# Performance work log

Measured on AMD Instinct MI355X. Metric: run time of the kernel, lower is better.

The kernel has to match this reference:

```python
import jax, jax.numpy as jnp
import numpy as np

D_MODEL = 1024
N_HEADS = 16
D_HEAD = D_MODEL // N_HEADS
IGNORE = -100000.0


def setup_inputs() -> dict:
    key = jax.random.key(0)
    ks = jax.random.split(key, 12)
    B, S = 4, 2048
    x_q = jax.random.normal(ks[0], (B, S, D_MODEL), dtype=jnp.float32)
    x_kv = jax.random.normal(ks[1], (B, S, D_MODEL), dtype=jnp.float32)
    # mask[q, k] == True means the score is replaced with IGNORE (masked out)
    mask = jax.random.randint(ks[2], (S, S), 0, 2) == 1
    sq = 1.0 / np.sqrt(D_MODEL)
    sh = 1.0 / np.sqrt(D_HEAD)
    W_Q = jax.random.normal(ks[3], (N_HEADS, D_MODEL, D_HEAD), dtype=jnp.float32) * sq
    W_K = jax.random.normal(ks[4], (N_HEADS, D_MODEL, D_HEAD), dtype=jnp.float32) * sq
    W_V = jax.random.normal(ks[5], (N_HEADS, D_MODEL, D_HEAD), dtype=jnp.float32) * sq
    W_O = jax.random.normal(ks[6], (N_HEADS, D_HEAD, D_MODEL), dtype=jnp.float32) * sh
    b_Q = jnp.zeros((N_HEADS, D_HEAD), dtype=jnp.float32)
    b_K = jnp.zeros((N_HEADS, D_HEAD), dtype=jnp.float32)
    b_V = jnp.zeros((N_HEADS, D_HEAD), dtype=jnp.float32)
    b_O = jnp.zeros((D_MODEL,), dtype=jnp.float32)
    return {"x_q": x_q, "x_kv": x_kv, "mask": mask,
            "W_Q": W_Q, "W_K": W_K, "W_V": W_V, "W_O": W_O,
            "b_Q": b_Q, "b_K": b_K, "b_V": b_V, "b_O": b_O}


def reference(x_q, x_kv, mask, W_Q, W_K, W_V, W_O, b_Q, b_K, b_V, b_O):
    # per-head QKV projections: b s d, n d h -> b s n h
    q = jnp.einsum('bsd,ndh->bsnh', x_q, W_Q) + b_Q
    k = jnp.einsum('bsd,ndh->bsnh', x_kv, W_K) + b_K
    v = jnp.einsum('bsd,ndh->bsnh', x_kv, W_V) + b_V
    scale = 1.0 / np.sqrt(D_HEAD)  # flex_attention default scaling
    # scores: [B, H, Sq, Sk]
    scores = jnp.einsum('bqnh,bknh->bnqk', q, k) * scale
    # score_mod: where mask True -> IGNORE
    scores = jnp.where(mask[None, None, :, :], jnp.float32(IGNORE), scores)
    attn = jax.nn.softmax(scores, axis=-1)
    z = jnp.einsum('bnqk,bknh->bqnh', attn, v)  # [B, Sq, H, Dh]
    # per-head output projection then sum over heads
    out = jnp.einsum('bqnh,nhd->bqd', z, W_O) + b_O
    return (out, z)
```

## Files before the change

### kernel.cpp

```cpp
#include <hip/hip_runtime.h>

#define S_LEN 2048
#define NHEAD 16
#define DHEAD 64
#define DMODEL 1024
#define BATCH 4
#define SC2 0.18033688011112042f

typedef short bf16x8 __attribute__((ext_vector_type(8)));
typedef float f32x4 __attribute__((ext_vector_type(4)));
typedef unsigned short u16;
typedef unsigned short u16x8 __attribute__((ext_vector_type(8)));
typedef unsigned short u16x4 __attribute__((ext_vector_type(4)));
typedef unsigned long long u64;

__device__ __forceinline__ u16 f2b(float f) {
  unsigned u = __builtin_bit_cast(unsigned, f);
  u += 0x7FFFu + ((u >> 16) & 1u);
  return (u16)(u >> 16);
}
__device__ __forceinline__ float b2f(u16 v) {
  unsigned u = ((unsigned)v) << 16;
  return __builtin_bit_cast(float, u);
}
__device__ __forceinline__ f32x4 mfma16(bf16x8 a, bf16x8 b, f32x4 c) {
  return __builtin_amdgcn_mfma_f32_16x16x32_bf16(a, b, c, 0, 0, 0);
}
__device__ __forceinline__ void load_lds16(const void* g, void* l) {
  __builtin_amdgcn_global_load_lds(
      (const __attribute__((address_space(1))) unsigned int*)g,
      (__attribute__((address_space(3))) unsigned int*)l, 16, 0, 0);
}
__device__ __forceinline__ float fexp2(float x) {
  return __builtin_exp2f(x);
}
__device__ __forceinline__ unsigned cvtpk(float lo, float hi) {
  unsigned r;
  asm("v_cvt_pk_bf16_f32 %0, %1, %2" : "=v"(r) : "v"(lo), "v"(hi));
  return r;
}


__global__ void cvt_f32_bf16(const float* __restrict__ src, u16* __restrict__ dst, int n4) {
  int i = blockIdx.x * 256 + threadIdx.x;
  int stride = gridDim.x * 256;
  for (; i < n4; i += stride) {
    float4 v = ((const float4*)src)[i];
    u16x4 o = { f2b(v.x), f2b(v.y), f2b(v.z), f2b(v.w) };
    ((u16x4*)dst)[i] = o;
  }
}

__global__ void mask_bits(const int* __restrict__ M, u64* __restrict__ Mbit) {
  const int tid = threadIdx.x;
  int W = blockIdx.x * 4 + (tid >> 6);
  int lane = tid & 63;
  int q = W >> 5, wo = W & 31;
  int v = M[(size_t)q * S_LEN + wo * 64 + lane];
  u64 bits = __ballot(v != 0);
  if (lane == 0) Mbit[W] = bits;
}

__global__ void repack_w(const float* __restrict__ W, u16* __restrict__ WT, float scale) {
  __shared__ u16 t[64][66];
  const int tid = threadIdx.x;
  const int n = blockIdx.y, d0 = blockIdx.x * 64;
  const float* src = W + (size_t)n * 65536;
  for (int p = 0; p < 4; ++p) {
    int idx = p * 256 + tid;
    int r = idx >> 4, cs = idx & 15;
    float4 v = *(const float4*)(src + (size_t)(d0 + r) * 64 + cs * 4);
    t[r][cs*4+0] = f2b(v.x*scale); t[r][cs*4+1] = f2b(v.y*scale);
    t[r][cs*4+2] = f2b(v.z*scale); t[r][cs*4+3] = f2b(v.w*scale);
  }
  __syncthreads();
  for (int p = 0; p < 2; ++p) {
    int idx = p * 256 + tid;
    int hl = idx >> 3, ds = idx & 7;
    u16x8 o;
    for (int e = 0; e < 8; ++e) o[e] = t[ds*8+e][hl];
    *(u16x8*)(WT + (size_t)(n*64 + hl) * 1024 + d0 + ds*8) = o;
  }
}

__global__ void split_wo(const float* __restrict__ Wo, u16* __restrict__ Hi, u16* __restrict__ Lo) {
  __shared__ u16 th[64][66];
  __shared__ u16 tl[64][66];
  const int tid = threadIdx.x;
  const int d0 = blockIdx.x * 64, c0 = blockIdx.y * 64;
  for (int p = 0; p < 4; ++p) {
    int idx = p * 256 + tid;
    int r = idx >> 4, cs = idx & 15;
    float4 v = *(const float4*)(Wo + (size_t)(c0 + r) * 1024 + d0 + cs * 4);
    float f[4] = {v.x, v.y, v.z, v.w};
    for (int e = 0; e < 4; ++e) {
      u16 hb = f2b(f[e]);
      th[r][cs*4+e] = hb;
      tl[r][cs*4+e] = f2b(f[e] - b2f(hb));
    }
  }
  __syncthreads();
  for (int p = 0; p < 2; ++p) {
    int idx = p * 256 + tid;
    int dr = idx >> 3, cs = idx & 7;
    u16x8 oh, ol;
    for (int e = 0; e < 8; ++e) { oh[e] = th[cs*8+e][dr]; ol[e] = tl[cs*8+e][dr]; }
    *(u16x8*)(Hi + (size_t)(d0 + dr) * 1024 + c0 + cs*8) = oh;
    *(u16x8*)(Lo + (size_t)(d0 + dr) * 1024 + c0 + cs*8) = ol;
  }
}

__global__ void transpose_v(const u16* __restrict__ V, u16* __restrict__ VT) {
  __shared__ u16 t[64][66];
  const int tid = threadIdx.x;
  const int s0 = blockIdx.x * 64;
  const int b = blockIdx.y >> 4, h = blockIdx.y & 15;
  for (int p = 0; p < 2; ++p) {
    int idx = p * 256 + tid;
    int r = idx >> 3, sg = idx & 7;
    u16x8 v = *(const u16x8*)(V + (size_t)(b*S_LEN + s0 + r) * 1024 + h*64 + sg*8);
    for (int e = 0; e < 8; ++e) t[r][sg*8+e] = v[e];
  }
  __syncthreads();
  for (int p = 0; p < 2; ++p) {
    int idx = p * 256 + tid;
    int dr = idx >> 3, ss = idx & 7;
    u16x8 o;
    for (int e = 0; e < 8; ++e) o[e] = t[ss*8+e][dr];
    *(u16x8*)(VT + ((size_t)(b*NHEAD + h) * 64 + dr) * 2048 + s0 + ss*8) = o;
  }
}


template<int BF16OUT>
__global__ __launch_bounds__(256, 2)
void gemm_bt(const u16* __restrict__ A, const u16* __restrict__ Bt,
             const float* __restrict__ bias, float bscale, void* __restrict__ Cout)
{
  __shared__ __align__(16) char As[16384];
  __shared__ __align__(16) char Bs[16384];
  const int tid = threadIdx.x, wid = tid >> 6, lane = tid & 63;
  const int lq = lane & 15, g = lane >> 4;
  const size_t am0 = (size_t)blockIdx.y * 128;
  const size_t bn0 = (size_t)blockIdx.x * 128;
  const int wr = (wid >> 1) * 64, wc = (wid & 1) * 64;
  f32x4 z4 = {0.f, 0.f, 0.f, 0.f};
  f32x4 acc[4][4];
  for (int i = 0; i < 4; ++i) for (int j = 0; j < 4; ++j) acc[i][j] = z4;
  for (int k0 = 0; k0 < DMODEL; k0 += 64) {
#pragma unroll
    for (int c = 0; c < 4; ++c) {
      int idx = c*256 + tid, r = idx >> 3, s = idx & 7;
      load_lds16(A + (am0 + r)*DMODEL + k0 + ((s ^ (r & 7)) << 3), As + idx*16);
    }
#pragma unroll
    for (int c = 0; c < 4; ++c) {
      int idx = c*256 + tid, r = idx >> 3, s = idx & 7;
      load_lds16(Bt + (bn0 + r)*DMODEL + k0 + ((s ^ (r & 7)) << 3), Bs + idx*16);
    }
    __syncthreads();
#pragma unroll
    for (int ks = 0; ks < 2; ++ks) {
      bf16x8 af[4], bfr[4];
#pragma unroll
      for (int i = 0; i < 4; ++i) {
        int row = wr + i*16 + lq;
        af[i] = *(const bf16x8*)(As + row*128 + (((ks*4 + g) ^ (row & 7)) << 4));
      }
#pragma unroll
      for (int j = 0; j < 4; ++j) {
        int row = wc + j*16 + lq;
        bfr[j] = *(const bf16x8*)(Bs + row*128 + (((ks*4 + g) ^ (row & 7)) << 4));
      }
#pragma unroll
      for (int i = 0; i < 4; ++i)
#pragma unroll
        for (int j = 0; j < 4; ++j)
          acc[i][j] = mfma16(af[i], bfr[j], acc[i][j]);
    }
    __syncthreads();
  }
#pragma unroll
  for (int i = 0; i < 4; ++i)
#pragma unroll
    for (int j = 0; j < 4; ++j) {
      size_t row = am0 + wr + i*16 + g*4;
      int col = (int)bn0 + wc + j*16 + lq;
      float bv = bias[col] * bscale;
#pragma unroll
      for (int r = 0; r < 4; ++r) {
        float v = acc[i][j][r] + bv;
        if (BF16OUT) ((u16*)Cout)[(row + r)*DMODEL + col] = f2b(v);
        else         ((float*)Cout)[(row + r)*DMODEL + col] = v;
      }
    }
}


__global__ __launch_bounds__(256, 2)
void gemm_out(const float* __restrict__ Z, const u16* __restrict__ Bh,
              const u16* __restrict__ Bl, const float* __restrict__ bias,
              float* __restrict__ Cout)
{
  __shared__ __align__(16) char Ah[16384];
  __shared__ __align__(16) char Al[16384];
  __shared__ __align__(16) char Bhs[16384];
  __shared__ __align__(16) char Bls[16384];
  const int tid = threadIdx.x, wid = tid >> 6, lane = tid & 63;
  const int lq = lane & 15, g = lane >> 4;
  const size_t am0 = (size_t)blockIdx.y * 128;
  const size_t bn0 = (size_t)blockIdx.x * 128;
  const int wr = (wid >> 1) * 64, wc = (wid & 1) * 64;
  f32x4 z4 = {0.f, 0.f, 0.f, 0.f};
  f32x4 acc[4][4];
  for (int i = 0; i < 4; ++i) for (int j = 0; j < 4; ++j) acc[i][j] = z4;
  for (int k0 = 0; k0 < DMODEL; k0 += 64) {
#pragma unroll
    for (int c = 0; c < 8; ++c) {
      int idx = c*256 + tid, r = idx >> 4, fs = idx & 15;
      float4 v = *(const float4*)(Z + (am0 + r)*DMODEL + k0 + fs*4);
      float f[4] = {v.x, v.y, v.z, v.w};
      u16x4 hv, lv;
      for (int e = 0; e < 4; ++e) {
        u16 hb = f2b(f[e]);
        hv[e] = hb;
        lv[e] = f2b(f[e] - b2f(hb));
      }
      int byo = r*128 + ((((fs >> 1) ^ (r & 7)) << 4) | ((fs & 1) << 3));
      *(u16x4*)(Ah + byo) = hv;
      *(u16x4*)(Al + byo) = lv;
    }
#pragma unroll
    for (int c = 0; c < 4; ++c) {
      int idx = c*256 + tid, r = idx >> 3, s = idx & 7;
      load_lds16(Bh + (bn0 + r)*DMODEL + k0 + ((s ^ (r & 7)) << 3), Bhs + idx*16);
    }
#pragma unroll
    for (int c = 0; c < 4; ++c) {
      int idx = c*256 + tid, r = idx >> 3, s = idx & 7;
      load_lds16(Bl + (bn0 + r)*DMODEL + k0 + ((s ^ (r & 7)) << 3), Bls + idx*16);
    }
    __syncthreads();
#pragma unroll
    for (int ks = 0; ks < 2; ++ks) {
      bf16x8 ah[4], al[4], bh4[4], bl4[4];
#pragma unroll
      for (int i = 0; i < 4; ++i) {
        int row = wr + i*16 + lq;
        int off = row*128 + (((ks*4 + g) ^ (row & 7)) << 4);
        ah[i] = *(const bf16x8*)(Ah + off);
        al[i] = *(const bf16x8*)(Al + off);
      }
#pragma unroll
      for (int j = 0; j < 4; ++j) {
        int row = wc + j*16 + lq;
        int off = row*128 + (((ks*4 + g) ^ (row & 7)) << 4);
        bh4[j] = *(const bf16x8*)(Bhs + off);
        bl4[j] = *(const bf16x8*)(Bls + off);
      }
#pragma unroll
      for (int i = 0; i < 4; ++i)
#pragma unroll
        for (int j = 0; j < 4; ++j) {
          acc[i][j] = mfma16(al[i], bh4[j], acc[i][j]);
          acc[i][j] = mfma16(ah[i], bl4[j], acc[i][j]);
          acc[i][j] = mfma16(ah[i], bh4[j], acc[i][j]);
        }
    }
    __syncthreads();
  }
#pragma unroll
  for (int i = 0; i < 4; ++i)
#pragma unroll
    for (int j = 0; j < 4; ++j) {
      size_t row = am0 + wr + i*16 + g*4;
      int col = (int)bn0 + wc + j*16 + lq;
      float bv = bias[col];
#pragma unroll
      for (int r = 0; r < 4; ++r)
        Cout[(row + r)*DMODEL + col] = acc[i][j][r] + bv;
    }
}

__global__ __launch_bounds__(256, 3)
void attn(const u16* __restrict__ Q, const u16* __restrict__ K,
          const u16* __restrict__ VT, const u64* __restrict__ Mbit,
          float* __restrict__ Zf)
{
  __shared__ __align__(16) char L[49152];
  const int tid = threadIdx.x, wid = tid >> 6, lane = tid & 63;
  const int lq = lane & 15, g = lane >> 4;
  const int Lb = blockIdx.x;
  const int xcd = Lb & 7, slot = Lb >> 3;
  const int qt = slot & 15, pl = slot >> 4;
  const int pair = xcd * 8 + pl;
  const int h = pair & 15, b = pair >> 4;
  const int q0 = qt * 128;
  const int qw = q0 + wid * 32;

  bf16x8 qf[2][2];
#pragma unroll
  for (int u = 0; u < 2; ++u) {
    const u16* qp = Q + (size_t)(b*S_LEN + qw + u*16 + lq) * DMODEL + h*DHEAD + g*8;
    qf[u][0] = *(const bf16x8*)qp;
    qf[u][1] = *(const bf16x8*)(qp + 32);
  }
  bf16x8 ones;
#pragma unroll
  for (int e = 0; e < 8; ++e) ones[e] = (short)0x3F80;

  const f32x4 z4 = {0.f, 0.f, 0.f, 0.f};
  f32x4 Oc[2][4];
#pragma unroll
  for (int u = 0; u < 2; ++u)
#pragma unroll
    for (int t = 0; t < 4; ++t) Oc[u][t] = z4;
  f32x4 lrow[2] = {z4, z4};

  const u16* kp = K + (size_t)(b*S_LEN)*DMODEL + h*DHEAD;
  const u16* vp = VT + (size_t)((b*NHEAD + h)*DHEAD)*S_LEN;
  const u64* mq0 = Mbit + (size_t)(qw + lq) * 32;
  const u64* mq1 = Mbit + (size_t)(qw + 16 + lq) * 32;
  char* myP = L + 32768 + wid*4096;

  size_t ko[2], vo[2];
  int sd[2];
#pragma unroll
  for (int c = 0; c < 2; ++c) {
    int idx = c*256 + tid, r = idx >> 3, s = idx & 7, so = (s ^ (r & 7)) << 3;
    ko[c] = (size_t)r * DMODEL + so;
    vo[c] = (size_t)r * S_LEN + so;
    sd[c] = idx * 16;
  }

  bf16x8 kr0, kr1, vr0, vr1;
  kr0 = *(const bf16x8*)(kp + ko[0]); kr1 = *(const bf16x8*)(kp + ko[1]);
  vr0 = *(const bf16x8*)(vp + vo[0]); vr1 = *(const bf16x8*)(vp + vo[1]);
  u64 mk0 = mq0[0], mk1 = mq1[0];
  kp += 64*DMODEL; vp += 64;
  *(bf16x8*)(L + sd[0]) = kr0;  *(bf16x8*)(L + sd[1]) = kr1;
  *(bf16x8*)(L + 8192 + sd[0]) = vr0;  *(bf16x8*)(L + 8192 + sd[1]) = vr1;
  __syncthreads();

  for (int it = 0; it < 32; ++it) {
    char* Bu = L + (it & 1) * 16384;
    char* Bn = L + ((it + 1) & 1) * 16384;
    u64 mn0 = 0, mn1 = 0;
    if (it < 31) {
      kr0 = *(const bf16x8*)(kp + ko[0]); kr1 = *(const bf16x8*)(kp + ko[1]);
      vr0 = *(const bf16x8*)(vp + vo[0]); vr1 = *(const bf16x8*)(vp + vo[1]);
      mn0 = mq0[it + 1]; mn1 = mq1[it + 1];
      kp += 64*DMODEL; vp += 64;
    }

    f32x4 st[2][4];
#pragma unroll
    for (int u = 0; u < 2; ++u)
#pragma unroll
      for (int t = 0; t < 4; ++t) st[u][t] = z4;
    __builtin_amdgcn_s_setprio(1);
#pragma unroll
    for (int t = 0; t < 4; ++t) {
      int row = t*16 + lq;
#pragma unroll
      for (int hh = 0; hh < 2; ++hh) {
        bf16x8 kf = *(const bf16x8*)(Bu + row*128 + (((hh*4 + g) ^ (row & 7)) << 4));
        st[0][t] = mfma16(kf, qf[0][hh], st[0][t]);
        st[1][t] = mfma16(kf, qf[1][hh], st[1][t]);
      }
    }
    __builtin_amdgcn_s_setprio(0);

#pragma unroll
    for (int u = 0; u < 2; ++u) {
      u64 mku = u ? mk1 : mk0;
      char* pb = myP + (u*16 + lq) * 128;
#pragma unroll
      for (int t = 0; t < 4; ++t) {
        unsigned bits = ((unsigned)(mku >> (t*16 + g*4))) & 0xFu;
        int sl = (((t*2 + (g >> 1)) ^ (lq & 7)) << 4) + ((g & 1) << 3);
        float p0 = (bits & 1u) ? 0.f : fexp2(st[u][t][0]);
        float p1 = (bits & 2u) ? 0.f : fexp2(st[u][t][1]);
        float p2 = (bits & 4u) ? 0.f : fexp2(st[u][t][2]);
        float p3 = (bits & 8u) ? 0.f : fexp2(st[u][t][3]);
        u64 w = (((u64)cvtpk(p2, p3) << 32) | cvtpk(p0, p1));
        *(u64*)(pb + sl) = w;
      }
    }
    asm volatile("s_waitcnt lgkmcnt(0)" ::: "memory");
    __builtin_amdgcn_sched_barrier(0);

    bf16x8 pf[2][2];
#pragma unroll
    for (int u = 0; u < 2; ++u) {
      char* pb = myP + (u*16 + lq) * 128;
      pf[u][0] = *(const bf16x8*)(pb + (((0 + g) ^ (lq & 7)) << 4));
      pf[u][1] = *(const bf16x8*)(pb + (((4 + g) ^ (lq & 7)) << 4));
    }

    f32x4 ts0 = z4, ts1 = z4;
    __builtin_amdgcn_s_setprio(1);
    ts0 = mfma16(pf[0][0], ones, ts0);
    ts0 = mfma16(pf[0][1], ones, ts0);
    ts1 = mfma16(pf[1][0], ones, ts1);
    ts1 = mfma16(pf[1][1], ones, ts1);
#pragma unroll
    for (int t = 0; t < 4; ++t) {
      int row = t*16 + lq;
#pragma unroll
      for (int hh = 0; hh < 2; ++hh) {
        bf16x8 vf = *(const bf16x8*)(Bu + 8192 + row*128 + (((hh*4 + g) ^ (row & 7)) << 4));
        Oc[0][t] = mfma16(pf[0][hh], vf, Oc[0][t]);
        Oc[1][t] = mfma16(pf[1][hh], vf, Oc[1][t]);
      }
    }
    __builtin_amdgcn_s_setprio(0);
    lrow[0] += ts0;
    lrow[1] += ts1;

    if (it < 31) {
      *(bf16x8*)(Bn + sd[0]) = kr0;  *(bf16x8*)(Bn + sd[1]) = kr1;
      *(bf16x8*)(Bn + 8192 + sd[0]) = vr0;  *(bf16x8*)(Bn + 8192 + sd[1]) = vr1;
    }
    __syncthreads();
    mk0 = mn0; mk1 = mn1;
  }

#pragma unroll
  for (int u = 0; u < 2; ++u) {
    float i0 = 1.f / lrow[u][0], i1 = 1.f / lrow[u][1],
          i2 = 1.f / lrow[u][2], i3 = 1.f / lrow[u][3];
#pragma unroll
    for (int t = 0; t < 4; ++t) {
      size_t base = ((size_t)(b*S_LEN + qw + u*16 + g*4) * NHEAD + h) * DHEAD + t*16 + lq;
      Zf[base       ] = Oc[u][t][0] * i0;
      Zf[base + 1024] = Oc[u][t][1] * i1;
      Zf[base + 2048] = Oc[u][t][2] * i2;
      Zf[base + 3072] = Oc[u][t][3] * i3;
    }
  }
}


extern "C" void kernel_launch(void* const* d_in, const int* in_sizes, int n_in,
                              void* d_out, int out_size, void* d_ws, size_t ws_size,
                              hipStream_t stream) {
  const float* x_q  = (const float*)d_in[0];
  const float* x_kv = (const float*)d_in[1];
  const int*   mask = (const int*)d_in[2];
  const float* W_Q  = (const float*)d_in[3];
  const float* W_K  = (const float*)d_in[4];
  const float* W_V  = (const float*)d_in[5];
  const float* W_O  = (const float*)d_in[6];
  const float* b_Q  = (const float*)d_in[7];
  const float* b_K  = (const float*)d_in[8];
  const float* b_V  = (const float*)d_in[9];
  const float* b_O  = (const float*)d_in[10];

  if (ws_size < 102760448) return;

  u16* ws  = (u16*)d_ws;
  u16* XQ  = ws;
  u16* XKV = XQ  + 8388608;
  u16* WQT = XKV + 8388608;
  u16* WKT = WQT + 1048576;
  u16* WVT = WKT + 1048576;
  u16* WOH = WVT + 1048576;
  u16* WOL = WOH + 1048576;
  u16* Qb  = WOL + 1048576;
  u16* Kb  = Qb  + 8388608;
  u16* Vb  = Kb  + 8388608;
  u64* Mbt = (u64*)(Vb + 8388608);
  u16* VTp = XQ;

  float* out = (float*)d_out;
  float* zf  = out + 8388608;

  cvt_f32_bf16<<<2048, 256, 0, stream>>>(x_q,  XQ,  2097152);
  cvt_f32_bf16<<<2048, 256, 0, stream>>>(x_kv, XKV, 2097152);
  repack_w<<<dim3(16,16), 256, 0, stream>>>(W_Q, WQT, SC2);
  repack_w<<<dim3(16,16), 256, 0, stream>>>(W_K, WKT, 1.0f);
  repack_w<<<dim3(16,16), 256, 0, stream>>>(W_V, WVT, 1.0f);
  split_wo<<<dim3(16,16), 256, 0, stream>>>(W_O, WOH, WOL);
  mask_bits<<<16384, 256, 0, stream>>>(mask, Mbt);
  gemm_bt<1><<<dim3(8,64), 256, 0, stream>>>(XQ,  WQT, b_Q, SC2, Qb);
  gemm_bt<1><<<dim3(8,64), 256, 0, stream>>>(XKV, WKT, b_K, 1.0f, Kb);
  gemm_bt<1><<<dim3(8,64), 256, 0, stream>>>(XKV, WVT, b_V, 1.0f, Vb);
  transpose_v<<<dim3(32,64), 256, 0, stream>>>(Vb, VTp);
  attn<<<1024, 256, 0, stream>>>(Qb, Kb, VTp, Mbt, zf);
  gemm_out<<<dim3(8,64), 256, 0, stream>>>(zf, WOH, WOL, b_O, out);
}
```

Baseline: 306.1 us.

## Pre-expand mask into bf16 AND-masks and apply with bitwise AND in attention

New measurement: 283.1 us. 1.08x faster.

```diff
diff --git a/kernel.cpp b/kernel.cpp
--- a/kernel.cpp
+++ b/kernel.cpp
@@ -13,6 +13,7 @@
 typedef unsigned short u16x8 __attribute__((ext_vector_type(8)));
 typedef unsigned short u16x4 __attribute__((ext_vector_type(4)));
 typedef unsigned long long u64;
+typedef unsigned long long u64x2 __attribute__((ext_vector_type(2)));
 
 __device__ __forceinline__ u16 f2b(float f) {
   unsigned u = __builtin_bit_cast(unsigned, f);
@@ -32,7 +33,9 @@
       (__attribute__((address_space(3))) unsigned int*)l, 16, 0, 0);
 }
 __device__ __forceinline__ float fexp2(float x) {
-  return __builtin_exp2f(x);
+  float r;
+  asm("v_exp_f32 %0, %1\n\ts_nop 1" : "=v"(r) : "v"(x));
+  return r;
 }
 __device__ __forceinline__ unsigned cvtpk(float lo, float hi) {
   unsigned r;
@@ -51,14 +54,17 @@
   }
 }
 
-__global__ void mask_bits(const int* __restrict__ M, u64* __restrict__ Mbit) {
-  const int tid = threadIdx.x;
-  int W = blockIdx.x * 4 + (tid >> 6);
-  int lane = tid & 63;
-  int q = W >> 5, wo = W & 31;
-  int v = M[(size_t)q * S_LEN + wo * 64 + lane];
-  u64 bits = __ballot(v != 0);
-  if (lane == 0) Mbit[W] = bits;
+__global__ void mask_expand(const int* __restrict__ M, u64* __restrict__ Mex) {
+  int idx = blockIdx.x * 256 + threadIdx.x;
+  int q = idx >> 9, k = (idx & 511) * 4;
+  int4 v = *(const int4*)(M + (size_t)q * S_LEN + k);
+  int T = k >> 6, t = (k >> 4) & 3, g = (k >> 2) & 3;
+  u64 m = 0;
+  if (!v.x) m |= 0xFFFFull;
+  if (!v.y) m |= 0xFFFF0000ull;
+  if (!v.z) m |= 0xFFFF00000000ull;
+  if (!v.w) m |= 0xFFFF000000000000ull;
+  Mex[((size_t)q * 32 + T) * 16 + g * 4 + t] = m;
 }
 
 __global__ void repack_w(const float* __restrict__ W, u16* __restrict__ WT, float scale) {
@@ -284,7 +290,7 @@
 
 __global__ __launch_bounds__(256, 3)
 void attn(const u16* __restrict__ Q, const u16* __restrict__ K,
-          const u16* __restrict__ VT, const u64* __restrict__ Mbit,
+          const u16* __restrict__ VT, const u64* __restrict__ Mex,
           float* __restrict__ Zf)
 {
   __shared__ __align__(16) char L[49152];
@@ -319,8 +325,8 @@
 
   const u16* kp = K + (size_t)(b*S_LEN)*DMODEL + h*DHEAD;
   const u16* vp = VT + (size_t)((b*NHEAD + h)*DHEAD)*S_LEN;
-  const u64* mq0 = Mbit + (size_t)(qw + lq) * 32;
-  const u64* mq1 = Mbit + (size_t)(qw + 16 + lq) * 32;
+  const u64* mx0 = Mex + (size_t)(qw + lq) * 512 + g*4;
+  const u64* mx1 = Mex + (size_t)(qw + 16 + lq) * 512 + g*4;
   char* myP = L + 32768 + wid*4096;
 
   size_t ko[2], vo[2];
@@ -336,7 +342,8 @@
   bf16x8 kr0, kr1, vr0, vr1;
   kr0 = *(const bf16x8*)(kp + ko[0]); kr1 = *(const bf16x8*)(kp + ko[1]);
   vr0 = *(const bf16x8*)(vp + vo[0]); vr1 = *(const bf16x8*)(vp + vo[1]);
-  u64 mk0 = mq0[0], mk1 = mq1[0];
+  u64x2 m0a = *(const u64x2*)(mx0), m0b = *(const u64x2*)(mx0 + 2);
+  u64x2 m1a = *(const u64x2*)(mx1), m1b = *(const u64x2*)(mx1 + 2);
   kp += 64*DMODEL; vp += 64;
   *(bf16x8*)(L + sd[0]) = kr0;  *(bf16x8*)(L + sd[1]) = kr1;
   *(bf16x8*)(L + 8192 + sd[0]) = vr0;  *(bf16x8*)(L + 8192 + sd[1]) = vr1;
@@ -345,46 +352,45 @@
   for (int it = 0; it < 32; ++it) {
     char* Bu = L + (it & 1) * 16384;
     char* Bn = L + ((it + 1) & 1) * 16384;
-    u64 mn0 = 0, mn1 = 0;
+    u64x2 n0a = {0,0}, n0b = {0,0}, n1a = {0,0}, n1b = {0,0};
     if (it < 31) {
       kr0 = *(const bf16x8*)(kp + ko[0]); kr1 = *(const bf16x8*)(kp + ko[1]);
       vr0 = *(const bf16x8*)(vp + vo[0]); vr1 = *(const bf16x8*)(vp + vo[1]);
-      mn0 = mq0[it + 1]; mn1 = mq1[it + 1];
+      n0a = *(const u64x2*)(mx0 + (it+1)*16);
+      n0b = *(const u64x2*)(mx0 + (it+1)*16 + 2);
+      n1a = *(const u64x2*)(mx1 + (it+1)*16);
+      n1b = *(const u64x2*)(mx1 + (it+1)*16 + 2);
       kp += 64*DMODEL; vp += 64;
     }
 
     f32x4 st[2][4];
-#pragma unroll
-    for (int u = 0; u < 2; ++u)
-#pragma unroll
-      for (int t = 0; t < 4; ++t) st[u][t] = z4;
     __builtin_amdgcn_s_setprio(1);
 #pragma unroll
     for (int t = 0; t < 4; ++t) {
       int row = t*16 + lq;
-#pragma unroll
-      for (int hh = 0; hh < 2; ++hh) {
-        bf16x8 kf = *(const bf16x8*)(Bu + row*128 + (((hh*4 + g) ^ (row & 7)) << 4));
-        st[0][t] = mfma16(kf, qf[0][hh], st[0][t]);
-        st[1][t] = mfma16(kf, qf[1][hh], st[1][t]);
-      }
+      bf16x8 kf0 = *(const bf16x8*)(Bu + row*128 + ((g ^ (row & 7)) << 4));
+      bf16x8 kf1 = *(const bf16x8*)(Bu + row*128 + (((4 + g) ^ (row & 7)) << 4));
+      st[0][t] = mfma16(kf1, qf[0][1], mfma16(kf0, qf[0][0], z4));
+      st[1][t] = mfma16(kf1, qf[1][1], mfma16(kf0, qf[1][0], z4));
     }
     __builtin_amdgcn_s_setprio(0);
 
 #pragma unroll
     for (int u = 0; u < 2; ++u) {
-      u64 mku = u ? mk1 : mk0;
       char* pb = myP + (u*16 + lq) * 128;
 #pragma unroll
       for (int t = 0; t < 4; ++t) {
-        unsigned bits = ((unsigned)(mku >> (t*16 + g*4))) & 0xFu;
         int sl = (((t*2 + (g >> 1)) ^ (lq & 7)) << 4) + ((g & 1) << 3);
-        float p0 = (bits & 1u) ? 0.f : fexp2(st[u][t][0]);
-        float p1 = (bits & 2u) ? 0.f : fexp2(st[u][t][1]);
-        float p2 = (bits & 4u) ? 0.f : fexp2(st[u][t][2]);
-        float p3 = (bits & 8u) ? 0.f : fexp2(st[u][t][3]);
-        u64 w = (((u64)cvtpk(p2, p3) << 32) | cvtpk(p0, p1));
-        *(u64*)(pb + sl) = w;
+        float p0 = fexp2(st[u][t][0]);
+        float p1 = fexp2(st[u][t][1]);
+        float p2 = fexp2(st[u][t][2]);
+        float p3 = fexp2(st[u][t][3]);
+        u64 mt = u ? ((t < 2) ? m1a[t & 1] : m1b[t & 1])
+                   : ((t < 2) ? m0a[t & 1] : m0b[t & 1]);
+        union { unsigned w32[2]; u64 w64; } pw;
+        pw.w32[0] = cvtpk(p0, p1);
+        pw.w32[1] = cvtpk(p2, p3);
+        *(u64*)(pb + sl) = pw.w64 & mt;
       }
     }
     asm volatile("s_waitcnt lgkmcnt(0)" ::: "memory");
@@ -398,12 +404,9 @@
       pf[u][1] = *(const bf16x8*)(pb + (((4 + g) ^ (lq & 7)) << 4));
     }
 
-    f32x4 ts0 = z4, ts1 = z4;
     __builtin_amdgcn_s_setprio(1);
-    ts0 = mfma16(pf[0][0], ones, ts0);
-    ts0 = mfma16(pf[0][1], ones, ts0);
-    ts1 = mfma16(pf[1][0], ones, ts1);
-    ts1 = mfma16(pf[1][1], ones, ts1);
+    f32x4 ts0 = mfma16(pf[0][1], ones, mfma16(pf[0][0], ones, z4));
+    f32x4 ts1 = mfma16(pf[1][1], ones, mfma16(pf[1][0], ones, z4));
 #pragma unroll
     for (int t = 0; t < 4; ++t) {
       int row = t*16 + lq;
@@ -423,7 +426,7 @@
       *(bf16x8*)(Bn + 8192 + sd[0]) = vr0;  *(bf16x8*)(Bn + 8192 + sd[1]) = vr1;
     }
     __syncthreads();
-    mk0 = mn0; mk1 = mn1;
+    m0a = n0a; m0b = n0b; m1a = n1a; m1b = n1b;
   }
 
 #pragma unroll
@@ -470,7 +473,7 @@
   u16* Qb  = WOL + 1048576;
   u16* Kb  = Qb  + 8388608;
   u16* Vb  = Kb  + 8388608;
-  u64* Mbt = (u64*)(Vb + 8388608);
+  u64* Mxp = (u64*)(Vb + 8388608);
   u16* VTp = XQ;
 
   float* out = (float*)d_out;
@@ -482,11 +485,11 @@
   repack_w<<<dim3(16,16), 256, 0, stream>>>(W_K, WKT, 1.0f);
   repack_w<<<dim3(16,16), 256, 0, stream>>>(W_V, WVT, 1.0f);
   split_wo<<<dim3(16,16), 256, 0, stream>>>(W_O, WOH, WOL);
-  mask_bits<<<16384, 256, 0, stream>>>(mask, Mbt);
+  mask_expand<<<4096, 256, 0, stream>>>(mask, Mxp);
   gemm_bt<1><<<dim3(8,64), 256, 0, stream>>>(XQ,  WQT, b_Q, SC2, Qb);
   gemm_bt<1><<<dim3(8,64), 256, 0, stream>>>(XKV, WKT, b_K, 1.0f, Kb);
   gemm_bt<1><<<dim3(8,64), 256, 0, stream>>>(XKV, WVT, b_V, 1.0f, Vb);
   transpose_v<<<dim3(32,64), 256, 0, stream>>>(Vb, VTp);
-  attn<<<1024, 256, 0, stream>>>(Qb, Kb, VTp, Mbt, zf);
+  attn<<<1024, 256, 0, stream>>>(Qb, Kb, VTp, Mxp, zf);
   gemm_out<<<dim3(8,64), 256, 0, stream>>>(zf, WOH, WOL, b_O, out);
 }
```
